# Kernel tuning notes

Hardware: AMD Instinct MI355X
Metric: run time of the kernel (lower is better)

## Reference

```python
import jax, jax.numpy as jnp
import numpy as np

B, C = 2, 2
D = H = W = 192
N_BIF = 64                 # bif ids 0..63; labels = bif*4 + stub (stub in 1..3)
NUM_LABELS = 4 * N_BIF     # 256
MIN_STUBS = 2
MIN_VOXELS = 1
TEMP = 0.2


def setup_inputs() -> dict:
    key = jax.random.key(0)
    k1, k2 = jax.random.split(key)
    pred = jax.random.normal(k1, (B, C, D, H, W), dtype=jnp.float32)
    stub_label_map = jax.random.randint(k2, (B, 1, D, H, W), 0, NUM_LABELS).astype(jnp.float32)
    return {"pred": pred, "stub_label_map": stub_label_map}


def reference(pred, stub_label_map):
    # foreground probability: softmax over channel dim, take class 1
    fg = jax.nn.softmax(pred, axis=1)[:, 1]                     # [B,D,H,W]
    labels = jnp.round(stub_label_map[:, 0]).astype(jnp.int32)  # [B,D,H,W]

    Bn = fg.shape[0]
    fg_flat = fg.reshape(Bn, -1)
    lab_flat = labels.reshape(Bn, -1)

    seg = lambda v, i: jax.ops.segment_sum(v, i, num_segments=NUM_LABELS)
    sums = jax.vmap(seg)(fg_flat, lab_flat)                      # [B, NUM_LABELS]
    counts = jax.vmap(seg)(jnp.ones_like(fg_flat), lab_flat)     # [B, NUM_LABELS]

    # group labels as [bif, stub]; drop bif 0 and stub 0 (never used in loop)
    sums = sums.reshape(Bn, N_BIF, 4)[:, 1:, 1:4]                # [B, N_BIF-1, 3]
    counts = counts.reshape(Bn, N_BIF, 4)[:, 1:, 1:4]

    valid = counts >= MIN_VOXELS                                 # stub has enough voxels
    means = sums / jnp.maximum(counts, 1.0)                      # per-stub mean fg prob

    # softmin over the valid stubs of each bif (masked softmax of -mean/temp)
    logits = jnp.where(valid, -means / TEMP, -1e9)
    weights = jax.nn.softmax(logits, axis=-1)
    score = jnp.sum(jnp.where(valid, means * weights, 0.0), axis=-1)  # [B, N_BIF-1]

    valid_bif = jnp.sum(valid, axis=-1) >= MIN_STUBS
    total = jnp.sum(jnp.where(valid_bif, 1.0 - score, 0.0))
    n_bifs = jnp.sum(valid_bif)
    return jnp.where(n_bifs > 0, total / jnp.maximum(n_bifs, 1).astype(total.dtype), 0.0)
```

## Files before the change

kernel.cpp:

```cpp
#include <hip/hip_runtime.h>
#include <math.h>

#define BATCH     2
#define NLAB      256
#define VOX       (192*192*192)
#define VVEC      (VOX/4)
#define TEMP      0.2f

#define STEP      4096.0f
#define INV_STEP  (1.0f/4096.0f)

__global__ __launch_bounds__(256) void histo_kernel(
    const float* __restrict__ pred,
    const float* __restrict__ labmap,
    float* __restrict__ ws_slots)
{
    __shared__ float s_hist[2 * NLAB];

    const int b = blockIdx.y;
    const int tid = threadIdx.x;

    s_hist[tid] = 0.0f;
    s_hist[tid + NLAB] = 0.0f;
    __syncthreads();

    const float4* p0 = (const float4*)(pred + (size_t)b * 2 * VOX);
    const float4* p1 = (const float4*)(pred + (size_t)b * 2 * VOX + VOX);
    const float4* lm = (const float4*)(labmap + (size_t)b * VOX);

    const int copy = (tid & 1) << 8;
    const int stride = gridDim.x * 256;
    for (int i = blockIdx.x * 256 + tid; i < VVEC; i += stride) {
        float4 a = p0[i];
        float4 c = p1[i];
        float4 l = lm[i];

        float fg0 = 1.0f / (1.0f + __expf(a.x - c.x));
        float fg1 = 1.0f / (1.0f + __expf(a.y - c.y));
        float fg2 = 1.0f / (1.0f + __expf(a.z - c.z));
        float fg3 = 1.0f / (1.0f + __expf(a.w - c.w));

        int l0 = ((int)(l.x + 0.5f)) & (NLAB - 1);
        int l1 = ((int)(l.y + 0.5f)) & (NLAB - 1);
        int l2 = ((int)(l.z + 0.5f)) & (NLAB - 1);
        int l3 = ((int)(l.w + 0.5f)) & (NLAB - 1);

        if ((l0 & 3) && l0 >= 4) atomicAdd(&s_hist[copy + l0], STEP + fg0);
        if ((l1 & 3) && l1 >= 4) atomicAdd(&s_hist[copy + l1], STEP + fg1);
        if ((l2 & 3) && l2 >= 4) atomicAdd(&s_hist[copy + l2], STEP + fg2);
        if ((l3 & 3) && l3 >= 4) atomicAdd(&s_hist[copy + l3], STEP + fg3);
    }
    __syncthreads();

    ws_slots[((size_t)(b * gridDim.x + blockIdx.x)) * NLAB + tid] =
        s_hist[tid] + s_hist[tid + NLAB];
}

__global__ __launch_bounds__(1024) void finalize_kernel(
    const float* __restrict__ ws_slots,
    int nslot,
    float* __restrict__ out)
{
    __shared__ float s_ps[BATCH][4][NLAB];
    __shared__ float s_pc[BATCH][4][NLAB];
    __shared__ float s_fsum[BATCH][NLAB];
    __shared__ float s_fcnt[BATCH][NLAB];

    const int tid  = threadIdx.x;
    const int bin  = tid & (NLAB - 1);
    const int part = tid >> 8;
    const int per  = (nslot + 3) >> 2;

    for (int b = 0; b < BATCH; ++b) {
        float cs = 0.0f, ss = 0.0f;
        int s0 = part * per;
        int s1 = s0 + per; if (s1 > nslot) s1 = nslot;
        for (int s = s0; s < s1; ++s) {
            float v = ws_slots[((size_t)(b * nslot + s)) * NLAB + bin];
            float c = floorf(v * INV_STEP + 0.5f);
            cs += c;
            ss += v - c * STEP;
        }
        s_ps[b][part][bin] = ss;
        s_pc[b][part][bin] = cs;
    }
    __syncthreads();

    if (tid < NLAB) {
        for (int b = 0; b < BATCH; ++b) {
            s_fsum[b][tid] = (s_ps[b][0][tid] + s_ps[b][1][tid])
                           + (s_ps[b][2][tid] + s_ps[b][3][tid]);
            s_fcnt[b][tid] = (s_pc[b][0][tid] + s_pc[b][1][tid])
                           + (s_pc[b][2][tid] + s_pc[b][3][tid]);
        }
    }
    __syncthreads();

    if (tid < 64) {
        float total = 0.0f;
        float nbifs = 0.0f;
        if (tid >= 1) {
            for (int bb = 0; bb < BATCH; ++bb) {
                float means[3];
                bool  valid[3];
                int   nvalid = 0;
                for (int s = 0; s < 3; ++s) {
                    int lab = tid * 4 + 1 + s;
                    float cnt = s_fcnt[bb][lab];
                    float sum = s_fsum[bb][lab];
                    valid[s] = (cnt >= 1.0f);
                    means[s] = sum / fmaxf(cnt, 1.0f);
                    nvalid  += valid[s] ? 1 : 0;
                }
                float logits[3], m = -3e38f;
                for (int s = 0; s < 3; ++s) {
                    logits[s] = valid[s] ? (-means[s] / TEMP) : -1e9f;
                    m = fmaxf(m, logits[s]);
                }
                float e[3], se = 0.0f;
                for (int s = 0; s < 3; ++s) { e[s] = __expf(logits[s] - m); se += e[s]; }
                float score = 0.0f;
                for (int s = 0; s < 3; ++s) {
                    if (valid[s]) score += means[s] * (e[s] / se);
                }
                if (nvalid >= 2) {
                    total += 1.0f - score;
                    nbifs += 1.0f;
                }
            }
        }
        for (int off = 32; off > 0; off >>= 1) {
            total += __shfl_down(total, off);
            nbifs += __shfl_down(nbifs, off);
        }
        if (tid == 0) {
            out[0] = (nbifs > 0.0f) ? (total / fmaxf(nbifs, 1.0f)) : 0.0f;
        }
    }
}

extern "C" void kernel_launch(void* const* d_in, const int* in_sizes, int n_in,
                              void* d_out, int out_size, void* d_ws, size_t ws_size,
                              hipStream_t stream) {
    const float* pred = (const float*)d_in[0];
    const float* lab  = (const float*)d_in[1];

    int gridx = 256;
    while ((size_t)gridx * BATCH * NLAB * sizeof(float) > ws_size && gridx > 8)
        gridx >>= 1;

    dim3 grid(gridx, BATCH);
    histo_kernel<<<grid, 256, 0, stream>>>(pred, lab, (float*)d_ws);
    finalize_kernel<<<1, 1024, 0, stream>>>((const float*)d_ws, gridx,
                                            (float*)d_out);
}
```

Baseline: 234.9 us.

## Split finalize into parallel multi-block reduce and scalar kernels, enlarge histogram grid

Raises the histogram grid from 256 to 1024 blocks per batch so more CUs are busy streaming the input. The single-block finalize, which would otherwise serially read four times as many slots, becomes a 32-block partial reduction followed by a small scalar kernel. This adds a third kernel launch and more workspace traffic in exchange for a wider histogram pass and a parallel slot reduction.

Result: faster. 225.1 us (-4.2%).

```diff
diff --git a/kernel.cpp b/kernel.cpp
--- a/kernel.cpp
+++ b/kernel.cpp
@@ -6,6 +6,7 @@
 #define VOX       (192*192*192)
 #define VVEC      (VOX/4)
 #define TEMP      0.2f
+#define NPART     16
 
 #define STEP      4096.0f
 #define INV_STEP  (1.0f/4096.0f)
@@ -56,43 +57,46 @@
         s_hist[tid] + s_hist[tid + NLAB];
 }
 
-__global__ __launch_bounds__(1024) void finalize_kernel(
+__global__ __launch_bounds__(256) void reduce_kernel(
     const float* __restrict__ ws_slots,
     int nslot,
+    float* __restrict__ psum,
+    float* __restrict__ pcnt)
+{
+    const int bin  = threadIdx.x;
+    const int b    = blockIdx.x / NPART;
+    const int part = blockIdx.x % NPART;
+    const int per  = nslot / NPART;
+
+    float cs = 0.0f, ss = 0.0f;
+    for (int s = part * per; s < (part + 1) * per; ++s) {
+        float v = ws_slots[((size_t)(b * nslot + s)) * NLAB + bin];
+        float c = floorf(v * INV_STEP + 0.5f);
+        cs += c;
+        ss += v - c * STEP;
+    }
+    psum[(size_t)blockIdx.x * NLAB + bin] = ss;
+    pcnt[(size_t)blockIdx.x * NLAB + bin] = cs;
+}
+
+__global__ __launch_bounds__(256) void scalar_kernel(
+    const float* __restrict__ psum,
+    const float* __restrict__ pcnt,
     float* __restrict__ out)
 {
-    __shared__ float s_ps[BATCH][4][NLAB];
-    __shared__ float s_pc[BATCH][4][NLAB];
     __shared__ float s_fsum[BATCH][NLAB];
     __shared__ float s_fcnt[BATCH][NLAB];
 
-    const int tid  = threadIdx.x;
-    const int bin  = tid & (NLAB - 1);
-    const int part = tid >> 8;
-    const int per  = (nslot + 3) >> 2;
+    const int tid = threadIdx.x;
 
     for (int b = 0; b < BATCH; ++b) {
-        float cs = 0.0f, ss = 0.0f;
-        int s0 = part * per;
-        int s1 = s0 + per; if (s1 > nslot) s1 = nslot;
-        for (int s = s0; s < s1; ++s) {
-            float v = ws_slots[((size_t)(b * nslot + s)) * NLAB + bin];
-            float c = floorf(v * INV_STEP + 0.5f);
-            cs += c;
-            ss += v - c * STEP;
+        float ss = 0.0f, cs = 0.0f;
+        for (int p = 0; p < NPART; ++p) {
+            ss += psum[(size_t)(b * NPART + p) * NLAB + tid];
+            cs += pcnt[(size_t)(b * NPART + p) * NLAB + tid];
         }
-        s_ps[b][part][bin] = ss;
-        s_pc[b][part][bin] = cs;
-    }
-    __syncthreads();
-
-    if (tid < NLAB) {
-        for (int b = 0; b < BATCH; ++b) {
-            s_fsum[b][tid] = (s_ps[b][0][tid] + s_ps[b][1][tid])
-                           + (s_ps[b][2][tid] + s_ps[b][3][tid]);
-            s_fcnt[b][tid] = (s_pc[b][0][tid] + s_pc[b][1][tid])
-                           + (s_pc[b][2][tid] + s_pc[b][3][tid]);
-        }
+        s_fsum[b][tid] = ss;
+        s_fcnt[b][tid] = cs;
     }
     __syncthreads();
 
@@ -145,12 +149,17 @@
     const float* pred = (const float*)d_in[0];
     const float* lab  = (const float*)d_in[1];
 
-    int gridx = 256;
-    while ((size_t)gridx * BATCH * NLAB * sizeof(float) > ws_size && gridx > 8)
+    int gridx = 1024;
+    while (((size_t)gridx * BATCH * NLAB + 2u * BATCH * NPART * NLAB) * sizeof(float)
+               > ws_size && gridx > NPART)
         gridx >>= 1;
 
+    float* ws_slots = (float*)d_ws;
+    float* psum = ws_slots + (size_t)BATCH * gridx * NLAB;
+    float* pcnt = psum + (size_t)BATCH * NPART * NLAB;
+
     dim3 grid(gridx, BATCH);
-    histo_kernel<<<grid, 256, 0, stream>>>(pred, lab, (float*)d_ws);
-    finalize_kernel<<<1, 1024, 0, stream>>>((const float*)d_ws, gridx,
-                                            (float*)d_out);
+    histo_kernel<<<grid, 256, 0, stream>>>(pred, lab, ws_slots);
+    reduce_kernel<<<BATCH * NPART, 256, 0, stream>>>(ws_slots, gridx, psum, pcnt);
+    scalar_kernel<<<1, 256, 0, stream>>>(psum, pcnt, (float*)d_out);
 }
```
